# Kernel optimization log

Measured on AMD Instinct MI355X. Metric: run time of the kernel, lower is better.

## Reference

```python
import jax, jax.numpy as jnp
import numpy as np

N = 100000   # nodes
E = 3200000  # directed edges
IN = 128     # in_channels
H = 16       # hidden_channels
OUT = 2      # out_channels
EPS = 1e-5   # BatchNorm eps


def setup_inputs() -> dict:
    key = jax.random.key(0)
    ks = jax.random.split(key, 16)
    x = jax.random.normal(ks[0], (N, IN), jnp.float32)
    edge_index = jax.random.randint(ks[1], (2, E), 0, N, jnp.int32)

    def lin(k, fan_in, fan_out):
        return jax.random.normal(k, (fan_in, fan_out), jnp.float32) / np.sqrt(fan_in)

    return {
        "x": x,
        "edge_index": edge_index,
        "W1": lin(ks[2], IN, H), "b1": jnp.zeros((H,), jnp.float32),
        "W2": lin(ks[3], H, H), "b2": jnp.zeros((H,), jnp.float32),
        "W3": lin(ks[4], H, H), "b3": jnp.zeros((H,), jnp.float32),
        "gamma1": jnp.ones((H,), jnp.float32), "beta1": jnp.zeros((H,), jnp.float32),
        "gamma2": jnp.ones((H,), jnp.float32), "beta2": jnp.zeros((H,), jnp.float32),
        "Wfc": lin(ks[5], H, OUT), "bfc": jnp.zeros((OUT,), jnp.float32),
    }


def reference(x, edge_index, W1, b1, W2, b2, W3, b3,
              gamma1, beta1, gamma2, beta2, Wfc, bfc):
    src, dst = edge_index[0], edge_index[1]
    # symmetric GCN normalization with self loops: deg includes +1 self loop
    deg = jax.ops.segment_sum(jnp.ones((E,), x.dtype), dst, num_segments=N) + 1.0
    dis = jax.lax.rsqrt(deg)                      # [N]
    norm = dis[src] * dis[dst]                    # [E]

    def gcn_conv(h, W, b):
        hw = h @ W                                # [N, F] dense transform
        msg = norm[:, None] * hw[src]             # gather + scale  [E, F]
        agg = jax.ops.segment_sum(msg, dst, num_segments=N)
        agg = agg + (dis * dis)[:, None] * hw     # self-loop contribution
        return agg + b

    def batch_norm(h, g, be):
        mu = h.mean(axis=0)
        var = h.var(axis=0)
        return (h - mu) * jax.lax.rsqrt(var + EPS) * g + be

    h = batch_norm(jax.nn.relu(gcn_conv(x, W1, b1)), gamma1, beta1)
    # dropout is identity in inference / deterministic reference
    h = batch_norm(jax.nn.relu(gcn_conv(h, W2, b2)), gamma2, beta2)
    h = gcn_conv(h, W3, b3)
    return jax.nn.log_softmax(h @ Wfc + bfc, axis=1)
```

## Files before the change

kernel.cpp:

```cpp
#include <hip/hip_runtime.h>
#include <hip/hip_fp16.h>

#define NN 100000
#define EE 3200000
#define INC 128
#define HC 16
#define BN_EPS 1e-5f

#define NPB 256
#define NBUCK ((NN + NPB - 1) / NPB)
#define CAP 9216
#define BINSZ ((size_t)NBUCK * CAP)
#define BTILE 4096
#define BGRID ((EE + BTILE - 1) / BTILE)
#define SB_CAP 12288

#define XSTR 132

__device__ __forceinline__ __half2 bits_to_h2(int v) { __half2 h; *(int*)&h = v; return h; }
__device__ __forceinline__ int h2_to_bits(__half2 h) { return *(int*)&h; }


__global__ void init_cursor(int* __restrict__ bcursor) {
    int k = blockIdx.x * blockDim.x + threadIdx.x;
    if (k < NBUCK) bcursor[k] = k * CAP;
}


__global__ void bin_edges(const int* __restrict__ src, const int* __restrict__ dst,
                          int* __restrict__ bcursor, unsigned* __restrict__ bin) {
    __shared__ unsigned stage[BTILE];
    __shared__ unsigned short sbuck[BTILE];
    __shared__ int hist[NBUCK], loff[NBUCK], gbase[NBUCK];
    __shared__ int sc[512];
    int tid = threadIdx.x;
    for (int k = tid; k < NBUCK; k += 512) hist[k] = 0;
    __syncthreads();
    int e0 = blockIdx.x * BTILE;
    int cnt = min(BTILE, EE - e0);
    for (int i = tid; i < cnt; i += 512) atomicAdd(&hist[dst[e0 + i] >> 8], 1);
    __syncthreads();
    int hv = (tid < NBUCK) ? hist[tid] : 0;
    sc[tid] = hv;
    __syncthreads();
    for (int off = 1; off < 512; off <<= 1) {
        int t = (tid >= off) ? sc[tid - off] : 0;
        __syncthreads();
        sc[tid] += t;
        __syncthreads();
    }
    if (tid < NBUCK) {
        loff[tid] = sc[tid] - hv;
        if (hv) gbase[tid] = atomicAdd(&bcursor[tid], hv);
    }
    __syncthreads();
    for (int k = tid; k < NBUCK; k += 512) hist[k] = 0;
    __syncthreads();
    for (int i = tid; i < cnt; i += 512) {
        int d = dst[e0 + i], s = src[e0 + i];
        int k = d >> 8;
        int p = loff[k] + atomicAdd(&hist[k], 1);
        stage[p] = ((unsigned)(d & 255) << 24) | (unsigned)s;
        sbuck[p] = (unsigned short)k;
    }
    __syncthreads();
    for (int i = tid; i < cnt; i += 512) {
        int k = sbuck[i];
        int idx = gbase[k] + (i - loff[k]);
        if (idx < (k + 1) * CAP) bin[idx] = stage[i];
    }
}


__global__ __launch_bounds__(512) void sort_bucket(const int* __restrict__ bcursor,
                            const unsigned* __restrict__ bin,
                            unsigned* __restrict__ bin2, unsigned* __restrict__ rowpack,
                            float* __restrict__ dis) {
    __shared__ unsigned stg[SB_CAP];
    __shared__ int cnt[NPB], pos[NPB], sc[NPB];
    int tid = threadIdx.x;
    for (int k = tid; k < NPB; k += 512) cnt[k] = 0;
    __syncthreads();
    int b = blockIdx.x;
    int beg = b * CAP;
    int n = min(bcursor[b], beg + CAP) - beg;
    for (int i = tid; i < n; i += 512) {
        unsigned u = bin[beg + i];
        if (i < SB_CAP) stg[i] = u;
        atomicAdd(&cnt[u >> 24], 1);
    }
    __syncthreads();
    int node = b * NPB + tid;
    int tot = 0;
    if (tid < NPB) {
        tot = cnt[tid] + ((node < NN) ? 1 : 0);
        sc[tid] = tot;
    }
    __syncthreads();
    for (int off = 1; off < NPB; off <<= 1) {
        int t = 0;
        if (tid < NPB && tid >= off) t = sc[tid - off];
        __syncthreads();
        if (tid < NPB) sc[tid] += t;
        __syncthreads();
    }
    if (tid < NPB) {
        int lo = sc[tid] - tot;
        if (node < NN) {
            bin2[beg + lo] = (unsigned)node;
            pos[tid] = lo + 1;
            rowpack[node] = ((unsigned)min(tot, 1023) << 22) | (unsigned)(beg + lo);
            dis[node] = rsqrtf((float)tot);
        } else {
            pos[tid] = lo;
        }
    }
    __syncthreads();
    for (int i = tid; i < n; i += 512) {
        unsigned u = (i < SB_CAP) ? stg[i] : bin[beg + i];
        int nl = u >> 24;
        int p = atomicAdd(&pos[nl], 1);
        bin2[beg + p] = u & 0xFFFFFFu;
    }
}


__global__ void gemm_x_w1(const float* __restrict__ x, const float* __restrict__ W1,
                          const float* __restrict__ dis, __half2* __restrict__ hws2) {
    __shared__ float Ws[INC * HC];
    __shared__ float xs[16 * XSTR];
    int tid = threadIdx.x;
    for (int i = tid; i < INC * HC; i += 256) Ws[i] = W1[i];
    int node0 = blockIdx.x * 16;
    const float4* xsrc = (const float4*)(x + (size_t)node0 * INC);
    float4* xdst = (float4*)xs;
    int nvalid = min(16, NN - node0);
    int nf4 = nvalid * 32;
    for (int i = tid; i < nf4; i += 256) {
        int nl = i >> 5, k4 = i & 31;
        xdst[nl * 33 + k4] = xsrc[i];
    }
    __syncthreads();
    int c = tid & 15;
    int nl = tid >> 4;
    int node = node0 + nl;
    if (node >= NN) return;
    const float* xr = xs + nl * XSTR;
    float sum = 0.f;
#pragma unroll
    for (int k = 0; k < INC; ++k) sum += xr[k] * Ws[k * 16 + c];
    sum *= dis[node];
    float other = __shfl_xor(sum, 1);
    if ((c & 1) == 0) hws2[node * 8 + (c >> 1)] = __floats2half2_rn(sum, other);
}

__global__ void gemm_bn_h_w(const float* __restrict__ agg, const float* __restrict__ stats,
                            const float* __restrict__ gamma, const float* __restrict__ beta,
                            const float* __restrict__ W, const float* __restrict__ dis,
                            __half2* __restrict__ hws2) {
    __shared__ float Ws[HC * HC];
    __shared__ float sc[HC], sf[HC];
    int tid = threadIdx.x;
    if (tid < HC * HC) Ws[tid] = W[tid];
    if (tid < HC) {
        const float invN = 1.0f / NN;
        float mu = stats[tid] * invN;
        float var = stats[16 + tid] * invN - mu * mu;
        float rs = rsqrtf(var + BN_EPS);
        sc[tid] = gamma[tid] * rs;
        sf[tid] = beta[tid] - mu * gamma[tid] * rs;
    }
    __syncthreads();
    int i = blockIdx.x * 256 + tid;
    if (i >= NN * HC) return;
    int n = i >> 4, c = i & 15;
    const float4* ar = (const float4*)(agg + n * HC);
    float sum = 0.f;
#pragma unroll
    for (int q = 0; q < 4; ++q) {
        float4 v = ar[q];
        int k = q * 4;
        float h0 = fmaxf(v.x, 0.f) * sc[k + 0] + sf[k + 0];
        float h1 = fmaxf(v.y, 0.f) * sc[k + 1] + sf[k + 1];
        float h2 = fmaxf(v.z, 0.f) * sc[k + 2] + sf[k + 2];
        float h3 = fmaxf(v.w, 0.f) * sc[k + 3] + sf[k + 3];
        sum += h0 * Ws[(k + 0) * 16 + c] + h1 * Ws[(k + 1) * 16 + c]
             + h2 * Ws[(k + 2) * 16 + c] + h3 * Ws[(k + 3) * 16 + c];
    }
    sum *= dis[n];
    float other = __shfl_xor(sum, 1);
    if ((c & 1) == 0) hws2[n * 8 + (c >> 1)] = __floats2half2_rn(sum, other);
}


__global__ void gcn_gather(const unsigned* __restrict__ rowpack,
                           const unsigned* __restrict__ bin2,
                           const __half2* __restrict__ hws2,
                           const float* __restrict__ b, float* __restrict__ agg) {
    int tid = threadIdx.x;
    int lane = tid & 63;
    int node = blockIdx.x * 4 + (tid >> 6);
    if (node >= NN) return;
    int cq = lane & 3;
    int slot = lane >> 2;
    unsigned rp = rowpack[node];
    int beg = (int)(rp & 0x3FFFFFu);
    int end = beg + (int)(rp >> 22);
    const char* hbase = (const char*)hws2;
    int e0 = beg + slot;
    int i0 = (e0      < end) ? (int)bin2[e0]      : NN;
    int i1 = (e0 + 16 < end) ? (int)bin2[e0 + 16] : NN;
    int i2 = (e0 + 32 < end) ? (int)bin2[e0 + 32] : NN;
    int2 h0 = *(const int2*)(hbase + ((size_t)(unsigned)i0 << 5) + cq * 8);
    int2 h1 = *(const int2*)(hbase + ((size_t)(unsigned)i1 << 5) + cq * 8);
    int2 h2 = *(const int2*)(hbase + ((size_t)(unsigned)i2 << 5) + cq * 8);
    __half2 accA = __hadd2(__hadd2(bits_to_h2(h0.x), bits_to_h2(h1.x)), bits_to_h2(h2.x));
    __half2 accB = __hadd2(__hadd2(bits_to_h2(h0.y), bits_to_h2(h1.y)), bits_to_h2(h2.y));
    for (int e = e0 + 48; e < end; e += 16) {
        int s = (int)bin2[e];
        int2 hv = *(const int2*)(hbase + ((size_t)(unsigned)s << 5) + cq * 8);
        accA = __hadd2(accA, bits_to_h2(hv.x));
        accB = __hadd2(accB, bits_to_h2(hv.y));
    }
    int ia = h2_to_bits(accA), ib = h2_to_bits(accB);
#pragma unroll
    for (int d = 4; d < 64; d <<= 1) {
        int oa = __shfl_xor(ia, d), ob = __shfl_xor(ib, d);
        accA = __hadd2(accA, bits_to_h2(oa));
        accB = __hadd2(accB, bits_to_h2(ob));
        ia = h2_to_bits(accA); ib = h2_to_bits(accB);
    }
    if (slot == 0) {
        float d = rsqrtf((float)(rp >> 22));
        float2 sa = __half22float2(accA), sb = __half22float2(accB);
        float4 r;
        r.x = d * sa.x + b[4 * cq + 0];
        r.y = d * sa.y + b[4 * cq + 1];
        r.z = d * sb.x + b[4 * cq + 2];
        r.w = d * sb.y + b[4 * cq + 3];
        ((float4*)agg)[node * 4 + cq] = r;
    }
}

__global__ void gather_fc(const unsigned* __restrict__ rowpack,
                          const unsigned* __restrict__ bin2,
                          const __half2* __restrict__ hws2,
                          const float* __restrict__ b, const float* __restrict__ Wfc,
                          const float* __restrict__ bfc, float* __restrict__ out) {
    int tid = threadIdx.x;
    int lane = tid & 63;
    int node = blockIdx.x * 4 + (tid >> 6);
    if (node >= NN) return;
    int cq = lane & 3;
    int slot = lane >> 2;
    unsigned rp = rowpack[node];
    int beg = (int)(rp & 0x3FFFFFu);
    int end = beg + (int)(rp >> 22);
    const char* hbase = (const char*)hws2;
    int e0 = beg + slot;
    int i0 = (e0      < end) ? (int)bin2[e0]      : NN;
    int i1 = (e0 + 16 < end) ? (int)bin2[e0 + 16] : NN;
    int i2 = (e0 + 32 < end) ? (int)bin2[e0 + 32] : NN;
    int2 h0 = *(const int2*)(hbase + ((size_t)(unsigned)i0 << 5) + cq * 8);
    int2 h1 = *(const int2*)(hbase + ((size_t)(unsigned)i1 << 5) + cq * 8);
    int2 h2 = *(const int2*)(hbase + ((size_t)(unsigned)i2 << 5) + cq * 8);
    __half2 accA = __hadd2(__hadd2(bits_to_h2(h0.x), bits_to_h2(h1.x)), bits_to_h2(h2.x));
    __half2 accB = __hadd2(__hadd2(bits_to_h2(h0.y), bits_to_h2(h1.y)), bits_to_h2(h2.y));
    for (int e = e0 + 48; e < end; e += 16) {
        int s = (int)bin2[e];
        int2 hv = *(const int2*)(hbase + ((size_t)(unsigned)s << 5) + cq * 8);
        accA = __hadd2(accA, bits_to_h2(hv.x));
        accB = __hadd2(accB, bits_to_h2(hv.y));
    }
    int ia = h2_to_bits(accA), ib = h2_to_bits(accB);
#pragma unroll
    for (int d = 4; d < 64; d <<= 1) {
        int oa = __shfl_xor(ia, d), ob = __shfl_xor(ib, d);
        accA = __hadd2(accA, bits_to_h2(oa));
        accB = __hadd2(accB, bits_to_h2(ob));
        ia = h2_to_bits(accA); ib = h2_to_bits(accB);
    }
    float z0 = 0.f, z1 = 0.f;
    if (slot == 0) {
        float d = rsqrtf((float)(rp >> 22));
        float2 sa = __half22float2(accA), sb = __half22float2(accB);
        float v0 = d * sa.x + b[4 * cq + 0];
        float v1 = d * sa.y + b[4 * cq + 1];
        float v2 = d * sb.x + b[4 * cq + 2];
        float v3 = d * sb.y + b[4 * cq + 3];
        int k = 4 * cq;
        z0 = v0 * Wfc[(k + 0) * 2 + 0] + v1 * Wfc[(k + 1) * 2 + 0]
           + v2 * Wfc[(k + 2) * 2 + 0] + v3 * Wfc[(k + 3) * 2 + 0];
        z1 = v0 * Wfc[(k + 0) * 2 + 1] + v1 * Wfc[(k + 1) * 2 + 1]
           + v2 * Wfc[(k + 2) * 2 + 1] + v3 * Wfc[(k + 3) * 2 + 1];
    }
    z0 += __shfl_xor(z0, 1); z1 += __shfl_xor(z1, 1);
    z0 += __shfl_xor(z0, 2); z1 += __shfl_xor(z1, 2);
    if (lane == 0) {
        z0 += bfc[0]; z1 += bfc[1];
        float m = fmaxf(z0, z1);
        float lse = m + logf(expf(z0 - m) + expf(z1 - m));
        out[node * 2 + 0] = z0 - lse;
        out[node * 2 + 1] = z1 - lse;
    }
}


__global__ void bn_stats_final(const float* __restrict__ agg, float* __restrict__ stats) {
    int tid = threadIdx.x;
    float s0 = 0.f, s1 = 0.f, s2 = 0.f, s3 = 0.f;
    float q0 = 0.f, q1 = 0.f, q2 = 0.f, q3 = 0.f;
    const float4* a4 = (const float4*)agg;
    const int n4 = NN * HC / 4;
    int i0 = blockIdx.x * 256 + tid;
    for (int i = i0; i < n4; i += gridDim.x * 256) {
        float4 v = a4[i];
        float r0 = fmaxf(v.x, 0.f), r1 = fmaxf(v.y, 0.f);
        float r2 = fmaxf(v.z, 0.f), r3 = fmaxf(v.w, 0.f);
        s0 += r0; s1 += r1; s2 += r2; s3 += r3;
        q0 += r0 * r0; q1 += r1 * r1; q2 += r2 * r2; q3 += r3 * r3;
    }
    int quad = i0 & 3;
    __shared__ float acc[32];
    if (tid < 32) acc[tid] = 0.f;
    __syncthreads();
    atomicAdd(&acc[4 * quad + 0], s0);
    atomicAdd(&acc[4 * quad + 1], s1);
    atomicAdd(&acc[4 * quad + 2], s2);
    atomicAdd(&acc[4 * quad + 3], s3);
    atomicAdd(&acc[16 + 4 * quad + 0], q0);
    atomicAdd(&acc[16 + 4 * quad + 1], q1);
    atomicAdd(&acc[16 + 4 * quad + 2], q2);
    atomicAdd(&acc[16 + 4 * quad + 3], q3);
    __syncthreads();
    if (tid < 32) atomicAdd(&stats[tid], acc[tid]);
}


extern "C" void kernel_launch(void* const* d_in, const int* in_sizes, int n_in,
                              void* d_out, int out_size, void* d_ws, size_t ws_size,
                              hipStream_t stream) {
    const float* x    = (const float*)d_in[0];
    const int*   ei   = (const int*)d_in[1];
    const int*   src  = ei;
    const int*   dstp = ei + EE;
    const float* W1   = (const float*)d_in[2];
    const float* b1   = (const float*)d_in[3];
    const float* W2   = (const float*)d_in[4];
    const float* b2   = (const float*)d_in[5];
    const float* W3   = (const float*)d_in[6];
    const float* b3   = (const float*)d_in[7];
    const float* g1   = (const float*)d_in[8];
    const float* be1  = (const float*)d_in[9];
    const float* g2   = (const float*)d_in[10];
    const float* be2  = (const float*)d_in[11];
    const float* Wfc  = (const float*)d_in[12];
    const float* bfc  = (const float*)d_in[13];
    float* out = (float*)d_out;

    char* p = (char*)d_ws;
    unsigned* bin   = (unsigned*)p;             p += BINSZ * 4;
    unsigned* bin2  = (unsigned*)p;             p += BINSZ * 4;
    __half2* hws2   = (__half2*)p;              p += (size_t)(NN + 1) * HC * 2;
    float*  agg     = (float*)p;                p += (size_t)NN * HC * 4;
    float*  dis     = (float*)p;                p += (size_t)NN * 4;
    unsigned* rowpack=(unsigned*)p;             p += (size_t)NN * 4;
    int*    bcursor = (int*)p;                  p += NBUCK * 4;
    float*  stats1  = (float*)p;                p += 32 * 4;
    float*  stats2  = (float*)p;                p += 32 * 4;

    const int TB = 256;
    const int gNH = (NN * HC + TB - 1) / TB;
    const int gX  = (NN + 15) / 16;
    const int gG  = (NN + 3) / 4;

    init_cursor<<<2, 256, 0, stream>>>(bcursor);
    hipMemsetAsync(stats1, 0, 64 * sizeof(float), stream);
    hipMemsetAsync(hws2 + (size_t)NN * 8, 0, HC * 2, stream);
    bin_edges<<<BGRID, 512, 0, stream>>>(src, dstp, bcursor, bin);
    sort_bucket<<<NBUCK, 512, 0, stream>>>(bcursor, bin, bin2, rowpack, dis);

    gemm_x_w1<<<gX, TB, 0, stream>>>(x, W1, dis, hws2);
    gcn_gather<<<gG, TB, 0, stream>>>(rowpack, bin2, hws2, b1, agg);
    bn_stats_final<<<1024, TB, 0, stream>>>(agg, stats1);

    gemm_bn_h_w<<<gNH, TB, 0, stream>>>(agg, stats1, g1, be1, W2, dis, hws2);
    gcn_gather<<<gG, TB, 0, stream>>>(rowpack, bin2, hws2, b2, agg);
    bn_stats_final<<<1024, TB, 0, stream>>>(agg, stats2);

    gemm_bn_h_w<<<gNH, TB, 0, stream>>>(agg, stats2, g2, be2, W3, dis, hws2);
    gather_fc<<<gG, TB, 0, stream>>>(rowpack, bin2, hws2, b3, Wfc, bfc, out);
}
```

Before: 266.8 us.

## Pad CSR rows to multiples of 48 with pre-shifted indices, sort in place

The bucket sort now writes the sorted adjacency back into the same bin buffer, dropping the second buffer. Each node's row is padded to a multiple of 48 with a sentinel pointing at a zero row, and indices are stored pre-shifted into byte offsets. This lets the gather kernels issue three unconditional loads per iteration with no bounds checks. The binning kernel also loads edges as int4 vectors and uses a wave-shuffle scan instead of a shared-memory scan. The cost is extra padded reads and writes, plus tighter limits on degree and per-bucket edge count.

Result: faster. 255.7 us (-4.1%).

```diff
diff --git a/kernel.cpp b/kernel.cpp
--- a/kernel.cpp
+++ b/kernel.cpp
@@ -9,8 +9,8 @@
 
 #define NPB 256
 #define NBUCK ((NN + NPB - 1) / NPB)
-#define CAP 9216
-#define BINSZ ((size_t)NBUCK * CAP)
+#define CAPU 13440
+#define BINSZ ((size_t)(NBUCK + 1) * CAPU)
 #define BTILE 4096
 #define BGRID ((EE + BTILE - 1) / BTILE)
 #define SB_CAP 12288
@@ -23,78 +23,121 @@
 
 __global__ void init_cursor(int* __restrict__ bcursor) {
     int k = blockIdx.x * blockDim.x + threadIdx.x;
-    if (k < NBUCK) bcursor[k] = k * CAP;
-}
-
-
-__global__ void bin_edges(const int* __restrict__ src, const int* __restrict__ dst,
+    if (k < NBUCK) bcursor[k] = k * CAPU;
+}
+
+
+__global__ __launch_bounds__(512) void bin_edges(const int* __restrict__ src,
+                          const int* __restrict__ dst,
                           int* __restrict__ bcursor, unsigned* __restrict__ bin) {
     __shared__ unsigned stage[BTILE];
     __shared__ unsigned short sbuck[BTILE];
     __shared__ int hist[NBUCK], loff[NBUCK], gbase[NBUCK];
-    __shared__ int sc[512];
-    int tid = threadIdx.x;
+    __shared__ int wsum[8];
+    int tid = threadIdx.x;
+    int lane = tid & 63, wid = tid >> 6;
     for (int k = tid; k < NBUCK; k += 512) hist[k] = 0;
     __syncthreads();
     int e0 = blockIdx.x * BTILE;
     int cnt = min(BTILE, EE - e0);
-    for (int i = tid; i < cnt; i += 512) atomicAdd(&hist[dst[e0 + i] >> 8], 1);
+    int n4 = cnt >> 2;
+    const int4* d4 = (const int4*)(dst + e0);
+    const int4* s4 = (const int4*)(src + e0);
+    int4 dv0 = {0,0,0,0}, dv1 = {0,0,0,0}, sv0 = {0,0,0,0}, sv1 = {0,0,0,0};
+    bool va0 = tid < n4, va1 = tid + 512 < n4;
+    if (va0) {
+        dv0 = d4[tid]; sv0 = s4[tid];
+        atomicAdd(&hist[dv0.x >> 8], 1);
+        atomicAdd(&hist[dv0.y >> 8], 1);
+        atomicAdd(&hist[dv0.z >> 8], 1);
+        atomicAdd(&hist[dv0.w >> 8], 1);
+    }
+    if (va1) {
+        dv1 = d4[tid + 512]; sv1 = s4[tid + 512];
+        atomicAdd(&hist[dv1.x >> 8], 1);
+        atomicAdd(&hist[dv1.y >> 8], 1);
+        atomicAdd(&hist[dv1.z >> 8], 1);
+        atomicAdd(&hist[dv1.w >> 8], 1);
+    }
     __syncthreads();
     int hv = (tid < NBUCK) ? hist[tid] : 0;
-    sc[tid] = hv;
-    __syncthreads();
-    for (int off = 1; off < 512; off <<= 1) {
-        int t = (tid >= off) ? sc[tid - off] : 0;
-        __syncthreads();
-        sc[tid] += t;
-        __syncthreads();
-    }
+    int v = hv;
+#pragma unroll
+    for (int off = 1; off < 64; off <<= 1) {
+        int t = __shfl_up(v, off);
+        if (lane >= off) v += t;
+    }
+    if (lane == 63) wsum[wid] = v;
+    __syncthreads();
+    if (tid == 0) {
+        int run = 0;
+#pragma unroll
+        for (int j = 0; j < 8; ++j) { int t = wsum[j]; wsum[j] = run; run += t; }
+    }
+    __syncthreads();
+    int excl = v - hv + wsum[wid];
     if (tid < NBUCK) {
-        loff[tid] = sc[tid] - hv;
+        loff[tid] = excl;
         if (hv) gbase[tid] = atomicAdd(&bcursor[tid], hv);
-    }
-    __syncthreads();
-    for (int k = tid; k < NBUCK; k += 512) hist[k] = 0;
-    __syncthreads();
-    for (int i = tid; i < cnt; i += 512) {
-        int d = dst[e0 + i], s = src[e0 + i];
-        int k = d >> 8;
-        int p = loff[k] + atomicAdd(&hist[k], 1);
-        stage[p] = ((unsigned)(d & 255) << 24) | (unsigned)s;
-        sbuck[p] = (unsigned short)k;
+        hist[tid] = 0;
+    }
+    __syncthreads();
+    {
+        int d, s, k, p;
+        if (va0) {
+            d = dv0.x; s = sv0.x; k = d >> 8; p = loff[k] + atomicAdd(&hist[k], 1);
+            stage[p] = ((unsigned)(d & 255) << 24) | (unsigned)s; sbuck[p] = (unsigned short)k;
+            d = dv0.y; s = sv0.y; k = d >> 8; p = loff[k] + atomicAdd(&hist[k], 1);
+            stage[p] = ((unsigned)(d & 255) << 24) | (unsigned)s; sbuck[p] = (unsigned short)k;
+            d = dv0.z; s = sv0.z; k = d >> 8; p = loff[k] + atomicAdd(&hist[k], 1);
+            stage[p] = ((unsigned)(d & 255) << 24) | (unsigned)s; sbuck[p] = (unsigned short)k;
+            d = dv0.w; s = sv0.w; k = d >> 8; p = loff[k] + atomicAdd(&hist[k], 1);
+            stage[p] = ((unsigned)(d & 255) << 24) | (unsigned)s; sbuck[p] = (unsigned short)k;
+        }
+        if (va1) {
+            d = dv1.x; s = sv1.x; k = d >> 8; p = loff[k] + atomicAdd(&hist[k], 1);
+            stage[p] = ((unsigned)(d & 255) << 24) | (unsigned)s; sbuck[p] = (unsigned short)k;
+            d = dv1.y; s = sv1.y; k = d >> 8; p = loff[k] + atomicAdd(&hist[k], 1);
+            stage[p] = ((unsigned)(d & 255) << 24) | (unsigned)s; sbuck[p] = (unsigned short)k;
+            d = dv1.z; s = sv1.z; k = d >> 8; p = loff[k] + atomicAdd(&hist[k], 1);
+            stage[p] = ((unsigned)(d & 255) << 24) | (unsigned)s; sbuck[p] = (unsigned short)k;
+            d = dv1.w; s = sv1.w; k = d >> 8; p = loff[k] + atomicAdd(&hist[k], 1);
+            stage[p] = ((unsigned)(d & 255) << 24) | (unsigned)s; sbuck[p] = (unsigned short)k;
+        }
     }
     __syncthreads();
     for (int i = tid; i < cnt; i += 512) {
         int k = sbuck[i];
         int idx = gbase[k] + (i - loff[k]);
-        if (idx < (k + 1) * CAP) bin[idx] = stage[i];
+        if (idx < k * CAPU + SB_CAP) bin[idx] = stage[i];
     }
 }
 
 
 __global__ __launch_bounds__(512) void sort_bucket(const int* __restrict__ bcursor,
-                            const unsigned* __restrict__ bin,
-                            unsigned* __restrict__ bin2, unsigned* __restrict__ rowpack,
-                            float* __restrict__ dis) {
+                            unsigned* __restrict__ bin,
+                            unsigned* __restrict__ rowpack, float* __restrict__ dis) {
     __shared__ unsigned stg[SB_CAP];
     __shared__ int cnt[NPB], pos[NPB], sc[NPB];
+    __shared__ int ptot_tot;
     int tid = threadIdx.x;
     for (int k = tid; k < NPB; k += 512) cnt[k] = 0;
     __syncthreads();
     int b = blockIdx.x;
-    int beg = b * CAP;
-    int n = min(bcursor[b], beg + CAP) - beg;
+    int beg = b * CAPU;
+    int n = min(bcursor[b] - beg, SB_CAP);
     for (int i = tid; i < n; i += 512) {
         unsigned u = bin[beg + i];
-        if (i < SB_CAP) stg[i] = u;
+        stg[i] = u;
         atomicAdd(&cnt[u >> 24], 1);
     }
     __syncthreads();
     int node = b * NPB + tid;
-    int tot = 0;
+    int tot = 0, ptot = 0;
     if (tid < NPB) {
         tot = cnt[tid] + ((node < NN) ? 1 : 0);
-        sc[tid] = tot;
+        ptot = ((tot + 47) / 48) * 48;
+        sc[tid] = ptot;
     }
     __syncthreads();
     for (int off = 1; off < NPB; off <<= 1) {
@@ -104,23 +147,27 @@
         if (tid < NPB) sc[tid] += t;
         __syncthreads();
     }
+    int lo = 0;
     if (tid < NPB) {
-        int lo = sc[tid] - tot;
+        lo = sc[tid] - ptot;
+        pos[tid] = lo + ((node < NN) ? 1 : 0);
+        if (tid == NPB - 1) ptot_tot = sc[tid];
         if (node < NN) {
-            bin2[beg + lo] = (unsigned)node;
-            pos[tid] = lo + 1;
-            rowpack[node] = ((unsigned)min(tot, 1023) << 22) | (unsigned)(beg + lo);
+            rowpack[node] = ((unsigned)min(tot, 511) << 23) | (unsigned)(beg + lo);
             dis[node] = rsqrtf((float)tot);
-        } else {
-            pos[tid] = lo;
         }
     }
     __syncthreads();
+    unsigned padv = (unsigned)NN << 5;
+    int fillN = ptot_tot;
+    for (int i = tid; i < fillN; i += 512) bin[beg + i] = padv;
+    __syncthreads();
+    if (tid < NPB && node < NN) bin[beg + lo] = (unsigned)node << 5;
     for (int i = tid; i < n; i += 512) {
-        unsigned u = (i < SB_CAP) ? stg[i] : bin[beg + i];
+        unsigned u = stg[i];
         int nl = u >> 24;
         int p = atomicAdd(&pos[nl], 1);
-        bin2[beg + p] = u & 0xFFFFFFu;
+        bin[beg + p] = (u & 0xFFFFFFu) << 5;
     }
 }
 
@@ -194,7 +241,7 @@
 
 
 __global__ void gcn_gather(const unsigned* __restrict__ rowpack,
-                           const unsigned* __restrict__ bin2,
+                           const unsigned* __restrict__ bin,
                            const __half2* __restrict__ hws2,
                            const float* __restrict__ b, float* __restrict__ agg) {
     int tid = threadIdx.x;
@@ -204,23 +251,23 @@
     int cq = lane & 3;
     int slot = lane >> 2;
     unsigned rp = rowpack[node];
-    int beg = (int)(rp & 0x3FFFFFu);
-    int end = beg + (int)(rp >> 22);
+    int beg = (int)(rp & 0x7FFFFFu);
+    int tot = (int)(rp >> 23);
     const char* hbase = (const char*)hws2;
     int e0 = beg + slot;
-    int i0 = (e0      < end) ? (int)bin2[e0]      : NN;
-    int i1 = (e0 + 16 < end) ? (int)bin2[e0 + 16] : NN;
-    int i2 = (e0 + 32 < end) ? (int)bin2[e0 + 32] : NN;
-    int2 h0 = *(const int2*)(hbase + ((size_t)(unsigned)i0 << 5) + cq * 8);
-    int2 h1 = *(const int2*)(hbase + ((size_t)(unsigned)i1 << 5) + cq * 8);
-    int2 h2 = *(const int2*)(hbase + ((size_t)(unsigned)i2 << 5) + cq * 8);
+    unsigned v0 = bin[e0], v1 = bin[e0 + 16], v2 = bin[e0 + 32];
+    int2 h0 = *(const int2*)(hbase + (size_t)v0 + cq * 8);
+    int2 h1 = *(const int2*)(hbase + (size_t)v1 + cq * 8);
+    int2 h2 = *(const int2*)(hbase + (size_t)v2 + cq * 8);
     __half2 accA = __hadd2(__hadd2(bits_to_h2(h0.x), bits_to_h2(h1.x)), bits_to_h2(h2.x));
     __half2 accB = __hadd2(__hadd2(bits_to_h2(h0.y), bits_to_h2(h1.y)), bits_to_h2(h2.y));
-    for (int e = e0 + 48; e < end; e += 16) {
-        int s = (int)bin2[e];
-        int2 hv = *(const int2*)(hbase + ((size_t)(unsigned)s << 5) + cq * 8);
-        accA = __hadd2(accA, bits_to_h2(hv.x));
-        accB = __hadd2(accB, bits_to_h2(hv.y));
+    for (int off = 48; off < tot; off += 48) {
+        unsigned w0 = bin[e0 + off], w1 = bin[e0 + off + 16], w2 = bin[e0 + off + 32];
+        int2 g0 = *(const int2*)(hbase + (size_t)w0 + cq * 8);
+        int2 g1 = *(const int2*)(hbase + (size_t)w1 + cq * 8);
+        int2 g2 = *(const int2*)(hbase + (size_t)w2 + cq * 8);
+        accA = __hadd2(accA, __hadd2(__hadd2(bits_to_h2(g0.x), bits_to_h2(g1.x)), bits_to_h2(g2.x)));
+        accB = __hadd2(accB, __hadd2(__hadd2(bits_to_h2(g0.y), bits_to_h2(g1.y)), bits_to_h2(g2.y)));
     }
     int ia = h2_to_bits(accA), ib = h2_to_bits(accB);
 #pragma unroll
@@ -231,7 +278,7 @@
         ia = h2_to_bits(accA); ib = h2_to_bits(accB);
     }
     if (slot == 0) {
-        float d = rsqrtf((float)(rp >> 22));
+        float d = rsqrtf((float)tot);
         float2 sa = __half22float2(accA), sb = __half22float2(accB);
         float4 r;
         r.x = d * sa.x + b[4 * cq + 0];
@@ -243,7 +290,7 @@
 }
 
 __global__ void gather_fc(const unsigned* __restrict__ rowpack,
-                          const unsigned* __restrict__ bin2,
+                          const unsigned* __restrict__ bin,
                           const __half2* __restrict__ hws2,
                           const float* __restrict__ b, const float* __restrict__ Wfc,
                           const float* __restrict__ bfc, float* __restrict__ out) {
@@ -254,23 +301,23 @@
     int cq = lane & 3;
     int slot = lane >> 2;
     unsigned rp = rowpack[node];
-    int beg = (int)(rp & 0x3FFFFFu);
-    int end = beg + (int)(rp >> 22);
+    int beg = (int)(rp & 0x7FFFFFu);
+    int tot = (int)(rp >> 23);
     const char* hbase = (const char*)hws2;
     int e0 = beg + slot;
-    int i0 = (e0      < end) ? (int)bin2[e0]      : NN;
-    int i1 = (e0 + 16 < end) ? (int)bin2[e0 + 16] : NN;
-    int i2 = (e0 + 32 < end) ? (int)bin2[e0 + 32] : NN;
-    int2 h0 = *(const int2*)(hbase + ((size_t)(unsigned)i0 << 5) + cq * 8);
-    int2 h1 = *(const int2*)(hbase + ((size_t)(unsigned)i1 << 5) + cq * 8);
-    int2 h2 = *(const int2*)(hbase + ((size_t)(unsigned)i2 << 5) + cq * 8);
+    unsigned v0 = bin[e0], v1 = bin[e0 + 16], v2 = bin[e0 + 32];
+    int2 h0 = *(const int2*)(hbase + (size_t)v0 + cq * 8);
+    int2 h1 = *(const int2*)(hbase + (size_t)v1 + cq * 8);
+    int2 h2 = *(const int2*)(hbase + (size_t)v2 + cq * 8);
     __half2 accA = __hadd2(__hadd2(bits_to_h2(h0.x), bits_to_h2(h1.x)), bits_to_h2(h2.x));
     __half2 accB = __hadd2(__hadd2(bits_to_h2(h0.y), bits_to_h2(h1.y)), bits_to_h2(h2.y));
-    for (int e = e0 + 48; e < end; e += 16) {
-        int s = (int)bin2[e];
-        int2 hv = *(const int2*)(hbase + ((size_t)(unsigned)s << 5) + cq * 8);
-        accA = __hadd2(accA, bits_to_h2(hv.x));
-        accB = __hadd2(accB, bits_to_h2(hv.y));
+    for (int off = 48; off < tot; off += 48) {
+        unsigned w0 = bin[e0 + off], w1 = bin[e0 + off + 16], w2 = bin[e0 + off + 32];
+        int2 g0 = *(const int2*)(hbase + (size_t)w0 + cq * 8);
+        int2 g1 = *(const int2*)(hbase + (size_t)w1 + cq * 8);
+        int2 g2 = *(const int2*)(hbase + (size_t)w2 + cq * 8);
+        accA = __hadd2(accA, __hadd2(__hadd2(bits_to_h2(g0.x), bits_to_h2(g1.x)), bits_to_h2(g2.x)));
+        accB = __hadd2(accB, __hadd2(__hadd2(bits_to_h2(g0.y), bits_to_h2(g1.y)), bits_to_h2(g2.y)));
     }
     int ia = h2_to_bits(accA), ib = h2_to_bits(accB);
 #pragma unroll
@@ -282,17 +329,17 @@
     }
     float z0 = 0.f, z1 = 0.f;
     if (slot == 0) {
-        float d = rsqrtf((float)(rp >> 22));
+        float d = rsqrtf((float)tot);
         float2 sa = __half22float2(accA), sb = __half22float2(accB);
-        float v0 = d * sa.x + b[4 * cq + 0];
-        float v1 = d * sa.y + b[4 * cq + 1];
-        float v2 = d * sb.x + b[4 * cq + 2];
-        float v3 = d * sb.y + b[4 * cq + 3];
+        float v0f = d * sa.x + b[4 * cq + 0];
+        float v1f = d * sa.y + b[4 * cq + 1];
+        float v2f = d * sb.x + b[4 * cq + 2];
+        float v3f = d * sb.y + b[4 * cq + 3];
         int k = 4 * cq;
-        z0 = v0 * Wfc[(k + 0) * 2 + 0] + v1 * Wfc[(k + 1) * 2 + 0]
-           + v2 * Wfc[(k + 2) * 2 + 0] + v3 * Wfc[(k + 3) * 2 + 0];
-        z1 = v0 * Wfc[(k + 0) * 2 + 1] + v1 * Wfc[(k + 1) * 2 + 1]
-           + v2 * Wfc[(k + 2) * 2 + 1] + v3 * Wfc[(k + 3) * 2 + 1];
+        z0 = v0f * Wfc[(k + 0) * 2 + 0] + v1f * Wfc[(k + 1) * 2 + 0]
+           + v2f * Wfc[(k + 2) * 2 + 0] + v3f * Wfc[(k + 3) * 2 + 0];
+        z1 = v0f * Wfc[(k + 0) * 2 + 1] + v1f * Wfc[(k + 1) * 2 + 1]
+           + v2f * Wfc[(k + 2) * 2 + 1] + v3f * Wfc[(k + 3) * 2 + 1];
     }
     z0 += __shfl_xor(z0, 1); z1 += __shfl_xor(z1, 1);
     z0 += __shfl_xor(z0, 2); z1 += __shfl_xor(z1, 2);
@@ -360,7 +407,6 @@
 
     char* p = (char*)d_ws;
     unsigned* bin   = (unsigned*)p;             p += BINSZ * 4;
-    unsigned* bin2  = (unsigned*)p;             p += BINSZ * 4;
     __half2* hws2   = (__half2*)p;              p += (size_t)(NN + 1) * HC * 2;
     float*  agg     = (float*)p;                p += (size_t)NN * HC * 4;
     float*  dis     = (float*)p;                p += (size_t)NN * 4;
@@ -378,16 +424,16 @@
     hipMemsetAsync(stats1, 0, 64 * sizeof(float), stream);
     hipMemsetAsync(hws2 + (size_t)NN * 8, 0, HC * 2, stream);
     bin_edges<<<BGRID, 512, 0, stream>>>(src, dstp, bcursor, bin);
-    sort_bucket<<<NBUCK, 512, 0, stream>>>(bcursor, bin, bin2, rowpack, dis);
+    sort_bucket<<<NBUCK, 512, 0, stream>>>(bcursor, bin, rowpack, dis);
 
     gemm_x_w1<<<gX, TB, 0, stream>>>(x, W1, dis, hws2);
-    gcn_gather<<<gG, TB, 0, stream>>>(rowpack, bin2, hws2, b1, agg);
+    gcn_gather<<<gG, TB, 0, stream>>>(rowpack, bin, hws2, b1, agg);
     bn_stats_final<<<1024, TB, 0, stream>>>(agg, stats1);
 
     gemm_bn_h_w<<<gNH, TB, 0, stream>>>(agg, stats1, g1, be1, W2, dis, hws2);
-    gcn_gather<<<gG, TB, 0, stream>>>(rowpack, bin2, hws2, b2, agg);
+    gcn_gather<<<gG, TB, 0, stream>>>(rowpack, bin, hws2, b2, agg);
     bn_stats_final<<<1024, TB, 0, stream>>>(agg, stats2);
 
     gemm_bn_h_w<<<gNH, TB, 0, stream>>>(agg, stats2, g2, be2, W3, dis, hws2);
-    gather_fc<<<gG, TB, 0, stream>>>(rowpack, bin2, hws2, b3, Wfc, bfc, out);
-}
+    gather_fc<<<gG, TB, 0, stream>>>(rowpack, bin, hws2, b3, Wfc, bfc, out);
+}
```
